# Kernel tuning notes

Hardware: AMD Instinct MI355X
Metric: run time of the kernel (lower is better)

## Reference

```python
import jax, jax.numpy as jnp
import numpy as np

# Fixed Grossberg constants (registered buffers in the torch module)
TAU = 0.8          # time constant
DECAY = 0.15       # passive decay A
B_CAP = 1.0        # excitatory cap B
C_FLOOR = 0.1      # inhibitory floor C
LAT_INHIB = 3.0    # lateral inhibition strength
DIV_SIGMA = 0.3    # divisive normalization sigma
ALPHA = 1.5        # excitatory gating alpha
BETA = 0.75        # inhibitory gating beta

BATCH = 32768
N = 17
T = 128
DT = 0.05


def _dynamics(state, W_pos, W_neg, feasibility, P):
    """Grossberg shunting ODE right-hand side. state: [B,17]."""
    # valences evaluated with environmental perturbation
    val_eval = state[:, 13:17] + P[:, 13:17]                       # [B,4]
    gate_exc = jax.nn.sigmoid(ALPHA * val_eval)                    # [B,4]
    gate_inh = jax.nn.sigmoid(-BETA * val_eval)                    # [B,4]
    ones9 = jnp.ones_like(state[:, :9])
    ones4 = jnp.ones_like(gate_exc)
    # gates expanded over nodes: only action nodes (9:13) gated
    ge_full = jnp.concatenate([ones9, gate_exc, ones4], axis=1)    # [B,17]
    gi_full = jnp.concatenate([ones9, gate_inh, ones4], axis=1)    # [B,17]
    # row-gating of W is equivalent to gating the matvec output
    exc = ge_full * jnp.einsum('bij,bj->bi', W_pos, state)         # [B,17]
    inh = gi_full * jnp.einsum('bij,bj->bi', W_neg, state)         # [B,17]
    E = jax.nn.relu(exc)
    I = jax.nn.relu(inh)
    # environmental drive routed through shunting terms for need nodes
    E_needs = E[:, :9] + jax.nn.relu(P[:, :9])
    I_needs = I[:, :9] + jax.nn.relu(-P[:, :9])
    # feasibility gates action excitation; selective lateral inhibition:
    # each action inhibited by the (divisively normalized) sum of OTHER actions
    acts = state[:, 9:13]
    other_sum = jnp.sum(acts, axis=1, keepdims=True) - acts
    lateral = LAT_INHIB * other_sum / (DIV_SIGMA + other_sum)
    E_acts = E[:, 9:13] * feasibility
    I_acts = I[:, 9:13] + lateral
    E_full = jnp.concatenate([E_needs, E_acts, E[:, 13:17]], axis=1)
    I_full = jnp.concatenate([I_needs, I_acts, I[:, 13:17]], axis=1)
    # direct additive perturbation only on valence nodes
    P_direct = jnp.concatenate([jnp.zeros_like(state[:, :13]), P[:, 13:17]], axis=1)
    return (-DECAY * state + (B_CAP - state) * E_full
            - (C_FLOOR + state) * I_full + P_direct) / TAU


def setup_inputs() -> dict:
    key = jax.random.key(0)
    k0, k1, k2, k3, k4 = jax.random.split(key, 5)
    state0 = jax.random.uniform(k0, (BATCH, N), dtype=jnp.float32)
    W_pos = 0.2 * jax.random.uniform(k1, (BATCH, N, N), dtype=jnp.float32)
    W_neg = 0.2 * jax.random.uniform(k2, (BATCH, N, N), dtype=jnp.float32)
    feasibility = jax.random.uniform(k3, (BATCH, 4), dtype=jnp.float32)
    perturbation = 0.1 * jax.random.normal(k4, (BATCH, N), dtype=jnp.float32)
    t_eval = jnp.arange(T, dtype=jnp.float32) * DT
    return {"state0": state0, "W_pos": W_pos, "W_neg": W_neg,
            "feasibility": feasibility, "perturbation": perturbation,
            "t_eval": t_eval}


def reference(state0, W_pos, W_neg, feasibility, perturbation, t_eval):
    dt = t_eval[1] - t_eval[0]
    n_steps = t_eval.shape[0] - 1  # static

    def step(s, _):
        ds = _dynamics(s, W_pos, W_neg, feasibility, perturbation)
        raw = s + dt * ds
        new = jnp.concatenate([
            jnp.clip(raw[:, 0:9], 0.0, 1.0),     # needs
            jnp.clip(raw[:, 9:13], 0.0, 1.0),    # actions
            jnp.clip(raw[:, 13:17], -1.0, 1.0),  # valences
        ], axis=1)
        return new, new

    _, traj = jax.lax.scan(step, state0, None, length=n_steps)
    return jnp.concatenate([state0[None], traj], axis=0)  # [T, B, 17]
```

## Files before the change

kernel.cpp:

```cpp
#include <hip/hip_runtime.h>


static constexpr int BATCH = 32768;
static constexpr int NN = 17;
static constexpr int TT = 128;

__global__ __launch_bounds__(256, 2) void hotco_kernel(
    const float* __restrict__ state0,
    const float* __restrict__ Wpos,
    const float* __restrict__ Wneg,
    const float* __restrict__ feas,
    const float* __restrict__ P,
    const float* __restrict__ t_eval,
    float* __restrict__ out)
{
    const int tid = blockIdx.x * blockDim.x + threadIdx.x;
    const int lane4 = tid & 3;
    const int b = tid >> 2;
    if (b >= BATCH) return;

    const int base = (lane4 == 0) ? 0 : (4 * lane4 + 1);
    const int nrows = (lane4 == 0) ? 5 : 4;

    float wp[5][17], wn[5][17];
    {
        const float* wpb = Wpos + (size_t)b * (NN * NN);
        const float* wnb = Wneg + (size_t)b * (NN * NN);
#pragma unroll
        for (int t = 0; t < 5; ++t) {
            if (t < nrows) {
                const float* rp = wpb + (base + t) * NN;
                const float* rn = wnb + (base + t) * NN;
#pragma unroll
                for (int j = 0; j < NN; ++j) { wp[t][j] = rp[j]; wn[t][j] = rn[j]; }
            } else {
#pragma unroll
                for (int j = 0; j < NN; ++j) { wp[t][j] = 0.f; wn[t][j] = 0.f; }
            }
        }
    }

    float s[17];
#pragma unroll
    for (int j = 0; j < NN; ++j) s[j] = state0[(size_t)b * NN + j];

    float sOwn[5];
#pragma unroll
    for (int t = 0; t < 5; ++t)
        sOwn[t] = (t < nrows) ? state0[(size_t)b * NN + base + t] : 0.f;

    float cA[5], cB[5];
    if (lane4 < 2) {
#pragma unroll
        for (int t = 0; t < 5; ++t) {
            float pv = P[(size_t)b * NN + base + t];
            cA[t] = fmaxf(pv, 0.f);
            cB[t] = fmaxf(-pv, 0.f);
        }
    } else if (lane4 == 2) {
#pragma unroll
        for (int t = 0; t < 4; ++t) {
            cA[t] = feas[(size_t)b * 4 + t];
            cB[t] = P[(size_t)b * NN + 13 + t];
        }
        cA[4] = 0.f; cB[4] = 0.f;
    } else {
#pragma unroll
        for (int t = 0; t < 4; ++t) {
            cA[t] = P[(size_t)b * NN + 13 + t];
            cB[t] = 0.f;
        }
        cA[4] = 0.f; cB[4] = 0.f;
    }

    const float lo = (lane4 == 3) ? -1.f : 0.f;
    const float dt = t_eval[1] - t_eval[0];
    const float k1 = dt / 0.8f;

    {
        float* op = out + (size_t)b * NN + base;
#pragma unroll
        for (int t = 0; t < 5; ++t)
            if (t < nrows) op[t] = sOwn[t];
    }

    float* outp = out + (size_t)BATCH * NN + (size_t)b * NN + base;

#pragma unroll 1
    for (int st = 1; st < TT; ++st) {
        float E5[5], I5[5];
#pragma unroll
        for (int t = 0; t < 5; ++t) {
            float ae = 0.f, ai = 0.f;
#pragma unroll
            for (int j = 0; j < NN; ++j) {
                ae = fmaf(wp[t][j], s[j], ae);
                ai = fmaf(wn[t][j], s[j], ai);
            }
            E5[t] = ae; I5[t] = ai;
        }

        if (lane4 == 2) {
            const float sum_acts = s[9] + s[10] + s[11] + s[12];
#pragma unroll
            for (int t = 0; t < 4; ++t) {
                float v  = s[13 + t] + cB[t];
                float ge = __builtin_amdgcn_rcpf(1.f + __expf(-1.5f * v));
                float gi = __builtin_amdgcn_rcpf(1.f + __expf(0.75f * v));
                float E  = fmaxf(ge * E5[t], 0.f) * cA[t];
                float os = sum_acts - s[9 + t];
                float lat = 3.0f * os * __builtin_amdgcn_rcpf(0.3f + os);
                float I  = fmaxf(gi * I5[t], 0.f) + lat;
                E5[t] = E; I5[t] = I;
            }
            E5[4] = 0.f; I5[4] = 0.f;
        } else if (lane4 == 3) {
#pragma unroll
            for (int t = 0; t < 5; ++t) {
                E5[t] = fmaxf(E5[t], 0.f);
                I5[t] = fmaxf(I5[t], 0.f);
            }
        } else {
#pragma unroll
            for (int t = 0; t < 5; ++t) {
                E5[t] = fmaxf(E5[t], 0.f) + cA[t];
                I5[t] = fmaxf(I5[t], 0.f) + cB[t];
            }
        }

        float ns[5];
#pragma unroll
        for (int t = 0; t < 5; ++t) {
            float so = sOwn[t];
            float pd = 0.f;
            if (t < 4) pd = (lane4 == 3) ? cA[t] : 0.f;
            float ds = fmaf(1.0f - so, E5[t], -0.15f * so)
                     - (0.1f + so) * I5[t] + pd;
            float raw = fmaf(k1, ds, so);
            ns[t] = fminf(fmaxf(raw, lo), 1.f);
            sOwn[t] = ns[t];
        }

#pragma unroll
        for (int j = 0; j < NN; ++j) {
            const int k = (j < 5) ? 0 : (j < 9) ? 1 : (j < 13) ? 2 : 3;
            const int c = (j < 5) ? j : (j < 9) ? (j - 5) : (j < 13) ? (j - 9) : (j - 13);
            s[j] = __shfl(ns[c], k, 4);
        }

#pragma unroll
        for (int t = 0; t < 5; ++t)
            if (t < nrows) outp[t] = ns[t];
        outp += (size_t)BATCH * NN;
    }
}

extern "C" void kernel_launch(void* const* d_in, const int* in_sizes, int n_in,
                              void* d_out, int out_size, void* d_ws, size_t ws_size,
                              hipStream_t stream) {
    const float* state0 = (const float*)d_in[0];
    const float* Wpos   = (const float*)d_in[1];
    const float* Wneg   = (const float*)d_in[2];
    const float* feasv  = (const float*)d_in[3];
    const float* P      = (const float*)d_in[4];
    const float* t_eval = (const float*)d_in[5];
    float* out = (float*)d_out;

    dim3 grid(BATCH * 4 / 256), block(256);
    hipLaunchKernelGGL(hotco_kernel, grid, block, 0, stream,
                       state0, Wpos, Wneg, feasv, P, t_eval, out);
}
```

Before: 172.0 us.

## Pack weights and state into fp16 pairs and use packed dot2 matvec

Weights and state are stored as packed half2 registers and the per-step matvec uses the fdot2 instruction, which halves the FMA count and the register footprint. State exchange between the four lanes now moves 9 packed words instead of 17 floats. The sigmoid gates are rewritten to share a single exp2, the lateral term is simplified algebraically, and the sum of actions is read from lane-local fp32 state. The trade is fp16 rounding of weights and state in the recurrent update, and the valence inputs to the gates are also read back from fp16. That precision loss can accumulate over 127 steps and may exceed the tolerance.

```diff
diff --git a/kernel.cpp b/kernel.cpp
--- a/kernel.cpp
+++ b/kernel.cpp
@@ -1,9 +1,28 @@
 #include <hip/hip_runtime.h>
-
+#include <stdint.h>
+
+
+typedef _Float16 h2 __attribute__((ext_vector_type(2)));
+typedef __fp16 h2raw __attribute__((ext_vector_type(2)));
 
 static constexpr int BATCH = 32768;
 static constexpr int NN = 17;
 static constexpr int TT = 128;
+
+__device__ __forceinline__ uint32_t pk(float a, float b) {
+    h2raw h = __builtin_amdgcn_cvt_pkrtz(a, b);
+    return __builtin_bit_cast(uint32_t, h);
+}
+
+__device__ __forceinline__ float dot2(uint32_t a, uint32_t b, float c) {
+#if __has_builtin(__builtin_amdgcn_fdot2)
+    return __builtin_amdgcn_fdot2(__builtin_bit_cast(h2, a),
+                                  __builtin_bit_cast(h2, b), c, false);
+#else
+    h2 ah = __builtin_bit_cast(h2, a), bh = __builtin_bit_cast(h2, b);
+    return c + (float)ah.x * (float)bh.x + (float)ah.y * (float)bh.y;
+#endif
+}
 
 __global__ __launch_bounds__(256, 2) void hotco_kernel(
     const float* __restrict__ state0,
@@ -22,7 +41,10 @@
     const int base = (lane4 == 0) ? 0 : (4 * lane4 + 1);
     const int nrows = (lane4 == 0) ? 5 : 4;
 
-    float wp[5][17], wn[5][17];
+    constexpr int pA[9] = {0, 2, 4, 5, 7, 9, 11, 13, 15};
+    constexpr int pB[9] = {1, 3, -1, 6, 8, 10, 12, 14, 16};
+
+    uint32_t wp[5][9], wn[5][9];
     {
         const float* wpb = Wpos + (size_t)b * (NN * NN);
         const float* wnb = Wneg + (size_t)b * (NN * NN);
@@ -32,50 +54,64 @@
                 const float* rp = wpb + (base + t) * NN;
                 const float* rn = wnb + (base + t) * NN;
 #pragma unroll
-                for (int j = 0; j < NN; ++j) { wp[t][j] = rp[j]; wn[t][j] = rn[j]; }
+                for (int c = 0; c < 9; ++c) {
+                    float a2 = (pB[c] < 0) ? 0.f : rp[pB[c]];
+                    float b2 = (pB[c] < 0) ? 0.f : rn[pB[c]];
+                    wp[t][c] = pk(rp[pA[c]], a2);
+                    wn[t][c] = pk(rn[pA[c]], b2);
+                }
             } else {
 #pragma unroll
-                for (int j = 0; j < NN; ++j) { wp[t][j] = 0.f; wn[t][j] = 0.f; }
-            }
-        }
-    }
-
-    float s[17];
-#pragma unroll
-    for (int j = 0; j < NN; ++j) s[j] = state0[(size_t)b * NN + j];
-
+                for (int c = 0; c < 9; ++c) { wp[t][c] = 0u; wn[t][c] = 0u; }
+            }
+        }
+    }
+
+    uint32_t s2[9];
+    {
+        float st[17];
+#pragma unroll
+        for (int j = 0; j < NN; ++j) st[j] = state0[(size_t)b * NN + j];
+#pragma unroll
+        for (int c = 0; c < 9; ++c)
+            s2[c] = pk(st[pA[c]], (pB[c] < 0) ? 0.f : st[pB[c]]);
+    }
     float sOwn[5];
 #pragma unroll
     for (int t = 0; t < 5; ++t)
         sOwn[t] = (t < nrows) ? state0[(size_t)b * NN + base + t] : 0.f;
 
-    float cA[5], cB[5];
+    float aE[5], aI[5], pdv[5];
+    float gP[4], gF[4];
+#pragma unroll
+    for (int t = 0; t < 5; ++t) { aE[t] = 0.f; aI[t] = 0.f; pdv[t] = 0.f; }
+#pragma unroll
+    for (int t = 0; t < 4; ++t) { gP[t] = 0.f; gF[t] = 0.f; }
     if (lane4 < 2) {
 #pragma unroll
         for (int t = 0; t < 5; ++t) {
-            float pv = P[(size_t)b * NN + base + t];
-            cA[t] = fmaxf(pv, 0.f);
-            cB[t] = fmaxf(-pv, 0.f);
+            if (t < nrows) {
+                float pv = P[(size_t)b * NN + base + t];
+                aE[t] = fmaxf(pv, 0.f);
+                aI[t] = fmaxf(-pv, 0.f);
+            }
         }
     } else if (lane4 == 2) {
 #pragma unroll
         for (int t = 0; t < 4; ++t) {
-            cA[t] = feas[(size_t)b * 4 + t];
-            cB[t] = P[(size_t)b * NN + 13 + t];
-        }
-        cA[4] = 0.f; cB[4] = 0.f;
+            gP[t] = P[(size_t)b * NN + 13 + t];
+            gF[t] = feas[(size_t)b * 4 + t];
+        }
     } else {
 #pragma unroll
-        for (int t = 0; t < 4; ++t) {
-            cA[t] = P[(size_t)b * NN + 13 + t];
-            cB[t] = 0.f;
-        }
-        cA[4] = 0.f; cB[4] = 0.f;
+        for (int t = 0; t < 4; ++t)
+            pdv[t] = P[(size_t)b * NN + 13 + t];
     }
 
     const float lo = (lane4 == 3) ? -1.f : 0.f;
     const float dt = t_eval[1] - t_eval[0];
     const float k1 = dt / 0.8f;
+    const float C  = -1.0820212806667226f;
 
     {
         float* op = out + (size_t)b * NN + base;
@@ -83,7 +119,6 @@
         for (int t = 0; t < 5; ++t)
             if (t < nrows) op[t] = sOwn[t];
     }
-
     float* outp = out + (size_t)BATCH * NN + (size_t)b * NN + base;
 
 #pragma unroll 1
@@ -93,64 +128,62 @@
         for (int t = 0; t < 5; ++t) {
             float ae = 0.f, ai = 0.f;
 #pragma unroll
-            for (int j = 0; j < NN; ++j) {
-                ae = fmaf(wp[t][j], s[j], ae);
-                ai = fmaf(wn[t][j], s[j], ai);
-            }
-            E5[t] = ae; I5[t] = ai;
+            for (int c = 0; c < 9; ++c) {
+                ae = dot2(wp[t][c], s2[c], ae);
+                ai = dot2(wn[t][c], s2[c], ai);
+            }
+            E5[t] = fmaxf(ae, 0.f);
+            I5[t] = fmaxf(ai, 0.f);
         }
 
         if (lane4 == 2) {
-            const float sum_acts = s[9] + s[10] + s[11] + s[12];
+            const float sum_acts = sOwn[0] + sOwn[1] + sOwn[2] + sOwn[3];
+            h2 q7 = __builtin_bit_cast(h2, s2[7]);
+            h2 q8 = __builtin_bit_cast(h2, s2[8]);
+            float v13[4] = { (float)q7.x, (float)q7.y, (float)q8.x, (float)q8.y };
 #pragma unroll
             for (int t = 0; t < 4; ++t) {
-                float v  = s[13 + t] + cB[t];
-                float ge = __builtin_amdgcn_rcpf(1.f + __expf(-1.5f * v));
-                float gi = __builtin_amdgcn_rcpf(1.f + __expf(0.75f * v));
-                float E  = fmaxf(ge * E5[t], 0.f) * cA[t];
-                float os = sum_acts - s[9 + t];
-                float lat = 3.0f * os * __builtin_amdgcn_rcpf(0.3f + os);
-                float I  = fmaxf(gi * I5[t], 0.f) + lat;
-                E5[t] = E; I5[t] = I;
+                float v  = v13[t] + gP[t];
+                float e1 = __builtin_amdgcn_exp2f(C * v);
+                float ge = __builtin_amdgcn_rcpf(fmaf(e1, e1, 1.f));
+                float gi = e1 * __builtin_amdgcn_rcpf(1.f + e1);
+                E5[t] = ge * E5[t] * gF[t];
+                float os  = sum_acts - sOwn[t];
+                float lat = fmaf(-0.9f, __builtin_amdgcn_rcpf(0.3f + os), 3.0f);
+                I5[t] = fmaf(gi, I5[t], lat);
             }
             E5[4] = 0.f; I5[4] = 0.f;
-        } else if (lane4 == 3) {
-#pragma unroll
-            for (int t = 0; t < 5; ++t) {
-                E5[t] = fmaxf(E5[t], 0.f);
-                I5[t] = fmaxf(I5[t], 0.f);
-            }
         } else {
 #pragma unroll
-            for (int t = 0; t < 5; ++t) {
-                E5[t] = fmaxf(E5[t], 0.f) + cA[t];
-                I5[t] = fmaxf(I5[t], 0.f) + cB[t];
-            }
-        }
-
-        float ns[5];
-#pragma unroll
-        for (int t = 0; t < 5; ++t) {
-            float so = sOwn[t];
-            float pd = 0.f;
-            if (t < 4) pd = (lane4 == 3) ? cA[t] : 0.f;
-            float ds = fmaf(1.0f - so, E5[t], -0.15f * so)
-                     - (0.1f + so) * I5[t] + pd;
-            float raw = fmaf(k1, ds, so);
-            ns[t] = fminf(fmaxf(raw, lo), 1.f);
-            sOwn[t] = ns[t];
-        }
-
-#pragma unroll
-        for (int j = 0; j < NN; ++j) {
-            const int k = (j < 5) ? 0 : (j < 9) ? 1 : (j < 13) ? 2 : 3;
-            const int c = (j < 5) ? j : (j < 9) ? (j - 5) : (j < 13) ? (j - 9) : (j - 13);
-            s[j] = __shfl(ns[c], k, 4);
-        }
+            for (int t = 0; t < 5; ++t) { E5[t] += aE[t]; I5[t] += aI[t]; }
+        }
+
+#pragma unroll
+        for (int t = 0; t < 5; ++t) {
+            float s  = sOwn[t];
+            float d0 = fmaf(-0.15f, s, pdv[t]);
+            float d1 = fmaf(1.f - s, E5[t], d0);
+            float d2 = fmaf(-(0.1f + s), I5[t], d1);
+            float raw = fmaf(k1, d2, s);
+            sOwn[t] = fminf(fmaxf(raw, lo), 1.f);
+        }
+
+        uint32_t pk0 = pk(sOwn[0], sOwn[1]);
+        uint32_t pk1 = pk(sOwn[2], sOwn[3]);
+        uint32_t pk2 = pk(sOwn[4], 0.f);
+        s2[0] = (uint32_t)__shfl((int)pk0, 0, 4);
+        s2[1] = (uint32_t)__shfl((int)pk1, 0, 4);
+        s2[2] = (uint32_t)__shfl((int)pk2, 0, 4);
+        s2[3] = (uint32_t)__shfl((int)pk0, 1, 4);
+        s2[4] = (uint32_t)__shfl((int)pk1, 1, 4);
+        s2[5] = (uint32_t)__shfl((int)pk0, 2, 4);
+        s2[6] = (uint32_t)__shfl((int)pk1, 2, 4);
+        s2[7] = (uint32_t)__shfl((int)pk0, 3, 4);
+        s2[8] = (uint32_t)__shfl((int)pk1, 3, 4);
 
 #pragma unroll
         for (int t = 0; t < 5; ++t)
-            if (t < nrows) outp[t] = ns[t];
+            if (t < nrows) outp[t] = sOwn[t];
         outp += (size_t)BATCH * NN;
     }
 }
```

Measured after the change: 147.6 us. 14.2% less time.
